# Kernel optimization log

Measured on AMD Instinct MI355X. Metric: run time of the kernel, lower is better.

## Reference

```python
import jax, jax.numpy as jnp
import numpy as np

B, D, E, T = 262144, 128, 8, 3   # batch, input_dim, num_experts, num_tasks
H1, H2, G = 64, 32, 64           # expert hidden dims, gate hidden dim


def setup_inputs() -> dict:
    key = jax.random.key(0)
    ks = jax.random.split(key, 9)
    s = 0.05
    return {
        "x":   jax.random.normal(ks[0], (B, D), dtype=jnp.float32),
        # stacked expert MLP params: D -> H1 (relu) -> H2 (relu)
        "We1": jax.random.normal(ks[1], (E, D, H1), dtype=jnp.float32) * s,
        "be1": jax.random.normal(ks[2], (E, H1), dtype=jnp.float32) * s,
        "We2": jax.random.normal(ks[3], (E, H1, H2), dtype=jnp.float32) * s,
        "be2": jax.random.normal(ks[4], (E, H2), dtype=jnp.float32) * s,
        # stacked gate MLP params: D -> G (relu) -> E (linear, then softmax)
        "Wg1": jax.random.normal(ks[5], (T, D, G), dtype=jnp.float32) * s,
        "bg1": jax.random.normal(ks[6], (T, G), dtype=jnp.float32) * s,
        "Wg2": jax.random.normal(ks[7], (T, G, E), dtype=jnp.float32) * s,
        "bg2": jax.random.normal(ks[8], (T, E), dtype=jnp.float32) * s,
    }


def reference(x, We1, be1, We2, be2, Wg1, bg1, Wg2, bg2):
    # All experts as one batched GEMM chain: [B,E,H1] -> [B,E,H2]
    h1 = jax.nn.relu(jnp.einsum('bd,edh->beh', x, We1) + be1)
    experts_out = jax.nn.relu(jnp.einsum('beh,eho->beo', h1, We2) + be2)  # [B,E,H2]
    # All task gates as one batched GEMM chain: [B,T,E]
    g = jax.nn.relu(jnp.einsum('bd,tdh->bth', x, Wg1) + bg1)
    gate = jax.nn.softmax(jnp.einsum('bth,the->bte', g, Wg2) + bg2, axis=-1)
    # softmax-weighted sum over experts, per task
    out = jnp.einsum('bte,beo->bto', gate, experts_out)  # [B,T,H2]
    return tuple(out[:, t] for t in range(T))
```

## Files before the change

kernel.cpp:

```cpp
#include <hip/hip_runtime.h>

#define BROWS 262144
#define OUT_TASK_F32 8388608

#define WS_L1F 0
#define WS_L2F 196608
#define WS_B1  235520
#define WS_B2  238592

#define H1B 0
#define EOB 24576
#define SGB 40960
#define XSB 42496
#define LDS_TOTAL 50688

typedef __attribute__((ext_vector_type(8))) short bf16x8;
typedef __attribute__((ext_vector_type(4))) float f32x4;
typedef __attribute__((ext_vector_type(2))) unsigned int u32x2;

#define MFMA16(a, b, c) __builtin_amdgcn_mfma_f32_16x16x32_bf16((a), (b), (c), 0, 0, 0)

__device__ __forceinline__ unsigned short f2bf(float f) {
  unsigned int u = __float_as_uint(f);
  return (unsigned short)((u + 0x7FFFu + ((u >> 16) & 1u)) >> 16);
}
__device__ __forceinline__ unsigned int cvtpk(float lo, float hi) {
  unsigned int r;
  asm("v_cvt_pk_bf16_f32 %0, %1, %2" : "=v"(r) : "v"(lo), "v"(hi));
  return r;
}

__global__ void pack_kernel(const float* __restrict__ We1, const float* __restrict__ be1,
                            const float* __restrict__ We2, const float* __restrict__ be2,
                            const float* __restrict__ Wg1, const float* __restrict__ bg1,
                            const float* __restrict__ Wg2, const float* __restrict__ bg2,
                            unsigned char* __restrict__ ws) {
  int idx = blockIdx.x * blockDim.x + threadIdx.x;
  unsigned short* L1F = (unsigned short*)(ws + WS_L1F);
  unsigned short* L2F = (unsigned short*)(ws + WS_L2F);
  float* B1 = (float*)(ws + WS_B1);
  float* B2 = (float*)(ws + WS_B2);
  if (idx < 98304) {
    int j = idx & 7, lane = (idx >> 3) & 63, ks = (idx >> 9) & 3, nt = idx >> 11;
    int k = ks * 32 + ((lane >> 4) << 3) + j;
    int n = nt * 16 + (lane & 15);
    float v = 0.f;
    if (n < 512)      v = We1[((n >> 6) * 128 + k) * 64 + (n & 63)];
    else if (n < 704) v = Wg1[(((n - 512) >> 6) * 128 + k) * 64 + ((n - 512) & 63)];
    L1F[idx] = f2bf(v);
  } else if (idx < 98304 + 19456) {
    int i2 = idx - 98304;
    int j = i2 & 7, lane = (i2 >> 3) & 63, ks = (i2 >> 9) & 1, nt = i2 >> 10;
    int k = ks * 32 + ((lane >> 4) << 3) + j;
    int n = nt * 16 + (lane & 15);
    float v = 0.f;
    if (n < 256) v = We2[((n >> 5) * 64 + k) * 32 + (n & 31)];
    else { int g = n - 256, t = g >> 4, eo = g & 15; if (eo < 8) v = Wg2[(t * 64 + k) * 8 + eo]; }
    L2F[i2] = f2bf(v);
  } else if (idx < 98304 + 19456 + 768) {
    int n = idx - (98304 + 19456);
    float v = 0.f;
    if (n < 512)      v = be1[n];
    else if (n < 704) v = bg1[n - 512];
    B1[n] = v;
  } else if (idx < 98304 + 19456 + 768 + 304) {
    int n = idx - (98304 + 19456 + 768);
    float v = 0.f;
    if (n < 256) v = be2[n];
    else { int g = n - 256, t = g >> 4, eo = g & 15; if (eo < 8) v = bg2[t * 8 + eo]; }
    B2[n] = v;
  }
}

__global__ __launch_bounds__(512, 2) void mmoe_kernel(const float* __restrict__ x,
                                                      const unsigned char* __restrict__ ws,
                                                      float* __restrict__ out) {
  __shared__ unsigned char lds[LDS_TOTAL];

  const int tid = threadIdx.x;
  const int l   = tid & 63;
  const int wid = tid >> 6;
  const int l15 = l & 15;
  const int lhi = l >> 4;
  const int swz = (l15 & 7) << 4;

  const bf16x8* L1F = (const bf16x8*)(ws + WS_L1F);
  const bf16x8* L2F = (const bf16x8*)(ws + WS_L2F);
  const float*  B1  = (const float*)(ws + WS_B1);
  const float*  B2  = (const float*)(ws + WS_B2);

  int ntb[6];
#pragma unroll
  for (int i = 0; i < 6; ++i) ntb[i] = wid * 6 + i;
  if (wid >= 6) {
    int b = wid - 6;
#pragma unroll
    for (int i = 0; i < 4; ++i) ntb[i] = 36 + b * 4 + i;
    ntb[4] = 44 + b * 2; ntb[5] = 45 + b * 2;
  }

  bf16x8 w1f[6][4];
  f32x4 b1v[6];
#pragma unroll
  for (int i = 0; i < 6; ++i) {
#pragma unroll
    for (int ks = 0; ks < 4; ++ks) w1f[i][ks] = L1F[(ntb[i] * 4 + ks) * 64 + l];
    b1v[i] = *(const f32x4*)(B1 + ntb[i] * 16 + lhi * 4);
  }
  bf16x8 w2f[2][2];
  f32x4 b2v[2];
#pragma unroll
  for (int i = 0; i < 2; ++i) {
#pragma unroll
    for (int ks = 0; ks < 2; ++ks) w2f[i][ks] = L2F[((wid * 2 + i) * 2 + ks) * 64 + l];
    b2v[i] = *(const f32x4*)(B2 + wid * 32 + i * 16 + lhi * 4);
  }
  bf16x8 wgf[2];
  f32x4 bgv = (f32x4){0.f, 0.f, 0.f, 0.f};
  if (wid >= 5) {
    int t = wid - 5;
#pragma unroll
    for (int ks = 0; ks < 2; ++ks) wgf[ks] = L2F[((16 + t) * 2 + ks) * 64 + l];
    bgv = *(const f32x4*)(B2 + 256 + t * 16 + lhi * 4);
  }

  const int srow = tid >> 5, sk4 = tid & 31;
  const int rowbase = blockIdx.x * 512;
  const int sswz = (srow & 7) << 4;

  {
    float4 sv = *(const float4*)(x + (size_t)(rowbase + srow) * 128 + sk4 * 4);
    u32x2 p; p[0] = cvtpk(sv.x, sv.y); p[1] = cvtpk(sv.z, sv.w);
    *(u32x2*)(lds + XSB + ((srow * 256 + sk4 * 8) ^ sswz)) = p;
  }
  __syncthreads();

  int cur = 0;
#pragma unroll 1
  for (int it = 0; it < 32; ++it) {
    float4 sv;
    const bool stage = (it + 1 < 32);
    if (stage)
      sv = *(const float4*)(x + (size_t)(rowbase + (it + 1) * 16 + srow) * 128 + sk4 * 4);

    if (it > 0 && wid < 6) {
      int t = wid >> 1, hf = wid & 1;
      f32x4 pA = *(const f32x4*)(lds + SGB + l15 * 96 + t * 32);
      f32x4 pB = *(const f32x4*)(lds + SGB + l15 * 96 + t * 32 + 16);
      f32x4 vac = (f32x4){0.f, 0.f, 0.f, 0.f};
#pragma unroll
      for (int e = 0; e < 4; ++e)
        vac += pA[e] * (*(const f32x4*)(lds + EOB + l15 * 1024 + ((e * 128 + hf * 64 + lhi * 16) ^ swz)));
#pragma unroll
      for (int e = 0; e < 4; ++e)
        vac += pB[e] * (*(const f32x4*)(lds + EOB + l15 * 1024 + (((e + 4) * 128 + hf * 64 + lhi * 16) ^ swz)));
      float* op = out + (size_t)t * OUT_TASK_F32 +
                  (size_t)(rowbase + (it - 1) * 16 + l15) * 32 + hf * 16 + lhi * 4;
      *(float4*)op = (float4){vac[0], vac[1], vac[2], vac[3]};
    }

    bf16x8 xa[4];
#pragma unroll
    for (int ks = 0; ks < 4; ++ks)
      xa[ks] = *(const bf16x8*)(lds + XSB + cur * 4096 + l15 * 256 + ((ks * 64 + lhi * 16) ^ swz));

    f32x4 acc[6];
#pragma unroll
    for (int i = 0; i < 6; ++i) acc[i] = b1v[i];
#pragma unroll
    for (int ks = 0; ks < 4; ++ks)
#pragma unroll
      for (int i = 0; i < 6; ++i)
        acc[i] = MFMA16(w1f[i][ks], xa[ks], acc[i]);

#pragma unroll
    for (int i = 0; i < 6; ++i) {
      float h0 = fmaxf(acc[i][0], 0.f), h1 = fmaxf(acc[i][1], 0.f);
      float h2 = fmaxf(acc[i][2], 0.f), h3 = fmaxf(acc[i][3], 0.f);
      u32x2 p; p[0] = cvtpk(h0, h1); p[1] = cvtpk(h2, h3);
      *(u32x2*)(lds + H1B + l15 * 1536 + ((ntb[i] * 32 + lhi * 8) ^ swz)) = p;
    }
    __syncthreads();

    bf16x8 hb0 = *(const bf16x8*)(lds + H1B + l15 * 1536 + ((wid * 128 + lhi * 16) ^ swz));
    bf16x8 hb1 = *(const bf16x8*)(lds + H1B + l15 * 1536 + ((wid * 128 + 64 + lhi * 16) ^ swz));
    f32x4 a2[2] = {b2v[0], b2v[1]};
#pragma unroll
    for (int i = 0; i < 2; ++i) {
      a2[i] = MFMA16(w2f[i][0], hb0, a2[i]);
      a2[i] = MFMA16(w2f[i][1], hb1, a2[i]);
      f32x4 r;
      r[0] = fmaxf(a2[i][0], 0.f); r[1] = fmaxf(a2[i][1], 0.f);
      r[2] = fmaxf(a2[i][2], 0.f); r[3] = fmaxf(a2[i][3], 0.f);
      *(f32x4*)(lds + EOB + l15 * 1024 + ((wid * 128 + i * 64 + lhi * 16) ^ swz)) = r;
    }

    if (wid >= 5) {
      int t = wid - 5;
      bf16x8 gb0 = *(const bf16x8*)(lds + H1B + l15 * 1536 + ((1024 + t * 128 + lhi * 16) ^ swz));
      bf16x8 gb1 = *(const bf16x8*)(lds + H1B + l15 * 1536 + ((1024 + t * 128 + 64 + lhi * 16) ^ swz));
      f32x4 ag = bgv;
      ag = MFMA16(wgf[0], gb0, ag);
      ag = MFMA16(wgf[1], gb1, ag);
      float s0 = ag[0], s1 = ag[1], s2 = ag[2], s3 = ag[3];
      float o0 = __shfl_xor(s0, 16), o1 = __shfl_xor(s1, 16);
      float o2 = __shfl_xor(s2, 16), o3 = __shfl_xor(s3, 16);
      float m = fmaxf(fmaxf(fmaxf(s0, s1), fmaxf(s2, s3)),
                      fmaxf(fmaxf(o0, o1), fmaxf(o2, o3)));
      float q0 = __expf(s0 - m), q1 = __expf(s1 - m), q2 = __expf(s2 - m), q3 = __expf(s3 - m);
      float ps = q0 + q1 + q2 + q3;
      float inv = 1.f / (ps + __shfl_xor(ps, 16));
      if (lhi < 2)
        *(f32x4*)(lds + SGB + l15 * 96 + t * 32 + lhi * 16) =
            (f32x4){q0 * inv, q1 * inv, q2 * inv, q3 * inv};
    }

    if (stage) {
      u32x2 p; p[0] = cvtpk(sv.x, sv.y); p[1] = cvtpk(sv.z, sv.w);
      *(u32x2*)(lds + XSB + (cur ^ 1) * 4096 + ((srow * 256 + sk4 * 8) ^ sswz)) = p;
    }
    __syncthreads();
    cur ^= 1;
  }

  if (wid < 6) {
    int t = wid >> 1, hf = wid & 1;
    f32x4 pA = *(const f32x4*)(lds + SGB + l15 * 96 + t * 32);
    f32x4 pB = *(const f32x4*)(lds + SGB + l15 * 96 + t * 32 + 16);
    f32x4 vac = (f32x4){0.f, 0.f, 0.f, 0.f};
#pragma unroll
    for (int e = 0; e < 4; ++e)
      vac += pA[e] * (*(const f32x4*)(lds + EOB + l15 * 1024 + ((e * 128 + hf * 64 + lhi * 16) ^ swz)));
#pragma unroll
    for (int e = 0; e < 4; ++e)
      vac += pB[e] * (*(const f32x4*)(lds + EOB + l15 * 1024 + (((e + 4) * 128 + hf * 64 + lhi * 16) ^ swz)));
    float* op = out + (size_t)t * OUT_TASK_F32 +
                (size_t)(rowbase + 31 * 16 + l15) * 32 + hf * 16 + lhi * 4;
    *(float4*)op = (float4){vac[0], vac[1], vac[2], vac[3]};
  }
}

extern "C" void kernel_launch(void* const* d_in, const int* in_sizes, int n_in,
                              void* d_out, int out_size, void* d_ws, size_t ws_size,
                              hipStream_t stream) {
  const float* x   = (const float*)d_in[0];
  const float* We1 = (const float*)d_in[1];
  const float* be1 = (const float*)d_in[2];
  const float* We2 = (const float*)d_in[3];
  const float* be2 = (const float*)d_in[4];
  const float* Wg1 = (const float*)d_in[5];
  const float* bg1 = (const float*)d_in[6];
  const float* Wg2 = (const float*)d_in[7];
  const float* bg2 = (const float*)d_in[8];
  unsigned char* ws = (unsigned char*)d_ws;
  float* out = (float*)d_out;

  pack_kernel<<<465, 256, 0, stream>>>(We1, be1, We2, be2, Wg1, bg1, Wg2, bg2, ws);
  mmoe_kernel<<<512, 512, 0, stream>>>(x, ws, out);
}
```

Baseline: 108.3 us.

## Process two 16-row sub-tiles per iteration to halve barriers per row

Each loop iteration now handles 32 rows as two 16-row MFMA sub-tiles, with the H1, expert-output, gate and x staging buffers all doubled in LDS. The grid drops from 512 to 256 blocks of 1024 rows each, and each thread stages 8 floats of x per iteration. The aim is to amortise the two __syncthreads per iteration and the loop overhead over twice as many rows, and to widen the x loads. In exchange, LDS use roughly doubles to about 99 KB, which may limit occupancy, and 256 blocks may not fill all CUs of the device.

```diff
diff --git a/kernel.cpp b/kernel.cpp
--- a/kernel.cpp
+++ b/kernel.cpp
@@ -9,14 +9,15 @@
 #define WS_B2  238592
 
 #define H1B 0
-#define EOB 24576
-#define SGB 40960
-#define XSB 42496
-#define LDS_TOTAL 50688
+#define EOB 49152
+#define SGB 81920
+#define XSB 84992
+#define LDS_TOTAL 101376
 
 typedef __attribute__((ext_vector_type(8))) short bf16x8;
 typedef __attribute__((ext_vector_type(4))) float f32x4;
 typedef __attribute__((ext_vector_type(2))) unsigned int u32x2;
+typedef __attribute__((ext_vector_type(4))) unsigned int u32x4;
 
 #define MFMA16(a, b, c) __builtin_amdgcn_mfma_f32_16x16x32_bf16((a), (b), (c), 0, 0, 0)
 
@@ -124,100 +125,116 @@
     bgv = *(const f32x4*)(B2 + 256 + t * 16 + lhi * 4);
   }
 
-  const int srow = tid >> 5, sk4 = tid & 31;
-  const int rowbase = blockIdx.x * 512;
-  const int sswz = (srow & 7) << 4;
+  const int r32 = tid >> 4;
+  const int c8  = (tid & 15) * 8;
+  const int sboff = (r32 >> 4) * 4096 + (r32 & 15) * 256 + (((tid & 15) * 16) ^ ((r32 & 7) << 4));
+  const int rowbase = blockIdx.x * 1024;
 
   {
-    float4 sv = *(const float4*)(x + (size_t)(rowbase + srow) * 128 + sk4 * 4);
-    u32x2 p; p[0] = cvtpk(sv.x, sv.y); p[1] = cvtpk(sv.z, sv.w);
-    *(u32x2*)(lds + XSB + ((srow * 256 + sk4 * 8) ^ sswz)) = p;
+    const float* xp = x + (size_t)(rowbase + r32) * 128 + c8;
+    float4 a = *(const float4*)xp, b = *(const float4*)(xp + 4);
+    u32x4 p; p[0] = cvtpk(a.x, a.y); p[1] = cvtpk(a.z, a.w);
+    p[2] = cvtpk(b.x, b.y); p[3] = cvtpk(b.z, b.w);
+    *(u32x4*)(lds + XSB + sboff) = p;
   }
   __syncthreads();
 
   int cur = 0;
 #pragma unroll 1
   for (int it = 0; it < 32; ++it) {
-    float4 sv;
+    float4 sa, sb;
     const bool stage = (it + 1 < 32);
-    if (stage)
-      sv = *(const float4*)(x + (size_t)(rowbase + (it + 1) * 16 + srow) * 128 + sk4 * 4);
+    if (stage) {
+      const float* xp = x + (size_t)(rowbase + (it + 1) * 32 + r32) * 128 + c8;
+      sa = *(const float4*)xp; sb = *(const float4*)(xp + 4);
+    }
 
     if (it > 0 && wid < 6) {
       int t = wid >> 1, hf = wid & 1;
-      f32x4 pA = *(const f32x4*)(lds + SGB + l15 * 96 + t * 32);
-      f32x4 pB = *(const f32x4*)(lds + SGB + l15 * 96 + t * 32 + 16);
-      f32x4 vac = (f32x4){0.f, 0.f, 0.f, 0.f};
-#pragma unroll
-      for (int e = 0; e < 4; ++e)
-        vac += pA[e] * (*(const f32x4*)(lds + EOB + l15 * 1024 + ((e * 128 + hf * 64 + lhi * 16) ^ swz)));
-#pragma unroll
-      for (int e = 0; e < 4; ++e)
-        vac += pB[e] * (*(const f32x4*)(lds + EOB + l15 * 1024 + (((e + 4) * 128 + hf * 64 + lhi * 16) ^ swz)));
-      float* op = out + (size_t)t * OUT_TASK_F32 +
-                  (size_t)(rowbase + (it - 1) * 16 + l15) * 32 + hf * 16 + lhi * 4;
-      *(float4*)op = (float4){vac[0], vac[1], vac[2], vac[3]};
-    }
-
-    bf16x8 xa[4];
-#pragma unroll
-    for (int ks = 0; ks < 4; ++ks)
-      xa[ks] = *(const bf16x8*)(lds + XSB + cur * 4096 + l15 * 256 + ((ks * 64 + lhi * 16) ^ swz));
-
-    f32x4 acc[6];
-#pragma unroll
-    for (int i = 0; i < 6; ++i) acc[i] = b1v[i];
-#pragma unroll
-    for (int ks = 0; ks < 4; ++ks)
-#pragma unroll
-      for (int i = 0; i < 6; ++i)
-        acc[i] = MFMA16(w1f[i][ks], xa[ks], acc[i]);
-
-#pragma unroll
-    for (int i = 0; i < 6; ++i) {
-      float h0 = fmaxf(acc[i][0], 0.f), h1 = fmaxf(acc[i][1], 0.f);
-      float h2 = fmaxf(acc[i][2], 0.f), h3 = fmaxf(acc[i][3], 0.f);
-      u32x2 p; p[0] = cvtpk(h0, h1); p[1] = cvtpk(h2, h3);
-      *(u32x2*)(lds + H1B + l15 * 1536 + ((ntb[i] * 32 + lhi * 8) ^ swz)) = p;
+#pragma unroll
+      for (int m = 0; m < 2; ++m) {
+        f32x4 pA = *(const f32x4*)(lds + SGB + m * 1536 + l15 * 96 + t * 32);
+        f32x4 pB = *(const f32x4*)(lds + SGB + m * 1536 + l15 * 96 + t * 32 + 16);
+        f32x4 vac = (f32x4){0.f, 0.f, 0.f, 0.f};
+#pragma unroll
+        for (int e = 0; e < 4; ++e)
+          vac += pA[e] * (*(const f32x4*)(lds + EOB + m * 16384 + l15 * 1024 +
+                                          ((e * 128 + hf * 64 + lhi * 16) ^ swz)));
+#pragma unroll
+        for (int e = 0; e < 4; ++e)
+          vac += pB[e] * (*(const f32x4*)(lds + EOB + m * 16384 + l15 * 1024 +
+                                          (((e + 4) * 128 + hf * 64 + lhi * 16) ^ swz)));
+        float* op = out + (size_t)t * OUT_TASK_F32 +
+                    (size_t)(rowbase + (it - 1) * 32 + m * 16 + l15) * 32 + hf * 16 + lhi * 4;
+        *(float4*)op = (float4){vac[0], vac[1], vac[2], vac[3]};
+      }
+    }
+
+#pragma unroll
+    for (int m = 0; m < 2; ++m) {
+      bf16x8 xa[4];
+#pragma unroll
+      for (int ks = 0; ks < 4; ++ks)
+        xa[ks] = *(const bf16x8*)(lds + XSB + cur * 8192 + m * 4096 + l15 * 256 +
+                                  ((ks * 64 + lhi * 16) ^ swz));
+      f32x4 acc[6];
+#pragma unroll
+      for (int i = 0; i < 6; ++i) acc[i] = b1v[i];
+#pragma unroll
+      for (int ks = 0; ks < 4; ++ks)
+#pragma unroll
+        for (int i = 0; i < 6; ++i)
+          acc[i] = MFMA16(w1f[i][ks], xa[ks], acc[i]);
+#pragma unroll
+      for (int i = 0; i < 6; ++i) {
+        u32x2 p;
+        p[0] = cvtpk(fmaxf(acc[i][0], 0.f), fmaxf(acc[i][1], 0.f));
+        p[1] = cvtpk(fmaxf(acc[i][2], 0.f), fmaxf(acc[i][3], 0.f));
+        *(u32x2*)(lds + H1B + m * 24576 + l15 * 1536 + ((ntb[i] * 32 + lhi * 8) ^ swz)) = p;
+      }
     }
     __syncthreads();
 
-    bf16x8 hb0 = *(const bf16x8*)(lds + H1B + l15 * 1536 + ((wid * 128 + lhi * 16) ^ swz));
-    bf16x8 hb1 = *(const bf16x8*)(lds + H1B + l15 * 1536 + ((wid * 128 + 64 + lhi * 16) ^ swz));
-    f32x4 a2[2] = {b2v[0], b2v[1]};
-#pragma unroll
-    for (int i = 0; i < 2; ++i) {
-      a2[i] = MFMA16(w2f[i][0], hb0, a2[i]);
-      a2[i] = MFMA16(w2f[i][1], hb1, a2[i]);
-      f32x4 r;
-      r[0] = fmaxf(a2[i][0], 0.f); r[1] = fmaxf(a2[i][1], 0.f);
-      r[2] = fmaxf(a2[i][2], 0.f); r[3] = fmaxf(a2[i][3], 0.f);
-      *(f32x4*)(lds + EOB + l15 * 1024 + ((wid * 128 + i * 64 + lhi * 16) ^ swz)) = r;
-    }
-
-    if (wid >= 5) {
-      int t = wid - 5;
-      bf16x8 gb0 = *(const bf16x8*)(lds + H1B + l15 * 1536 + ((1024 + t * 128 + lhi * 16) ^ swz));
-      bf16x8 gb1 = *(const bf16x8*)(lds + H1B + l15 * 1536 + ((1024 + t * 128 + 64 + lhi * 16) ^ swz));
-      f32x4 ag = bgv;
-      ag = MFMA16(wgf[0], gb0, ag);
-      ag = MFMA16(wgf[1], gb1, ag);
-      float s0 = ag[0], s1 = ag[1], s2 = ag[2], s3 = ag[3];
-      float o0 = __shfl_xor(s0, 16), o1 = __shfl_xor(s1, 16);
-      float o2 = __shfl_xor(s2, 16), o3 = __shfl_xor(s3, 16);
-      float m = fmaxf(fmaxf(fmaxf(s0, s1), fmaxf(s2, s3)),
-                      fmaxf(fmaxf(o0, o1), fmaxf(o2, o3)));
-      float q0 = __expf(s0 - m), q1 = __expf(s1 - m), q2 = __expf(s2 - m), q3 = __expf(s3 - m);
-      float ps = q0 + q1 + q2 + q3;
-      float inv = 1.f / (ps + __shfl_xor(ps, 16));
-      if (lhi < 2)
-        *(f32x4*)(lds + SGB + l15 * 96 + t * 32 + lhi * 16) =
-            (f32x4){q0 * inv, q1 * inv, q2 * inv, q3 * inv};
+#pragma unroll
+    for (int m = 0; m < 2; ++m) {
+      bf16x8 hb0 = *(const bf16x8*)(lds + H1B + m * 24576 + l15 * 1536 + ((wid * 128 + lhi * 16) ^ swz));
+      bf16x8 hb1 = *(const bf16x8*)(lds + H1B + m * 24576 + l15 * 1536 + ((wid * 128 + 64 + lhi * 16) ^ swz));
+      f32x4 a2[2] = {b2v[0], b2v[1]};
+#pragma unroll
+      for (int i = 0; i < 2; ++i) {
+        a2[i] = MFMA16(w2f[i][0], hb0, a2[i]);
+        a2[i] = MFMA16(w2f[i][1], hb1, a2[i]);
+        f32x4 r;
+        r[0] = fmaxf(a2[i][0], 0.f); r[1] = fmaxf(a2[i][1], 0.f);
+        r[2] = fmaxf(a2[i][2], 0.f); r[3] = fmaxf(a2[i][3], 0.f);
+        *(f32x4*)(lds + EOB + m * 16384 + l15 * 1024 + ((wid * 128 + i * 64 + lhi * 16) ^ swz)) = r;
+      }
+
+      if (wid >= 5) {
+        int t = wid - 5;
+        bf16x8 gb0 = *(const bf16x8*)(lds + H1B + m * 24576 + l15 * 1536 + ((1024 + t * 128 + lhi * 16) ^ swz));
+        bf16x8 gb1 = *(const bf16x8*)(lds + H1B + m * 24576 + l15 * 1536 + ((1024 + t * 128 + 64 + lhi * 16) ^ swz));
+        f32x4 ag = bgv;
+        ag = MFMA16(wgf[0], gb0, ag);
+        ag = MFMA16(wgf[1], gb1, ag);
+        float s0 = ag[0], s1 = ag[1], s2 = ag[2], s3 = ag[3];
+        float o0 = __shfl_xor(s0, 16), o1 = __shfl_xor(s1, 16);
+        float o2 = __shfl_xor(s2, 16), o3 = __shfl_xor(s3, 16);
+        float mx = fmaxf(fmaxf(fmaxf(s0, s1), fmaxf(s2, s3)),
+                         fmaxf(fmaxf(o0, o1), fmaxf(o2, o3)));
+        float q0 = __expf(s0 - mx), q1 = __expf(s1 - mx), q2 = __expf(s2 - mx), q3 = __expf(s3 - mx);
+        float ps = q0 + q1 + q2 + q3;
+        float inv = 1.f / (ps + __shfl_xor(ps, 16));
+        if (lhi < 2)
+          *(f32x4*)(lds + SGB + m * 1536 + l15 * 96 + t * 32 + lhi * 16) =
+              (f32x4){q0 * inv, q1 * inv, q2 * inv, q3 * inv};
+      }
     }
 
     if (stage) {
-      u32x2 p; p[0] = cvtpk(sv.x, sv.y); p[1] = cvtpk(sv.z, sv.w);
-      *(u32x2*)(lds + XSB + (cur ^ 1) * 4096 + ((srow * 256 + sk4 * 8) ^ sswz)) = p;
+      u32x4 p; p[0] = cvtpk(sa.x, sa.y); p[1] = cvtpk(sa.z, sa.w);
+      p[2] = cvtpk(sb.x, sb.y); p[3] = cvtpk(sb.z, sb.w);
+      *(u32x4*)(lds + XSB + (cur ^ 1) * 8192 + sboff) = p;
     }
     __syncthreads();
     cur ^= 1;
@@ -225,18 +242,23 @@
 
   if (wid < 6) {
     int t = wid >> 1, hf = wid & 1;
-    f32x4 pA = *(const f32x4*)(lds + SGB + l15 * 96 + t * 32);
-    f32x4 pB = *(const f32x4*)(lds + SGB + l15 * 96 + t * 32 + 16);
-    f32x4 vac = (f32x4){0.f, 0.f, 0.f, 0.f};
-#pragma unroll
-    for (int e = 0; e < 4; ++e)
-      vac += pA[e] * (*(const f32x4*)(lds + EOB + l15 * 1024 + ((e * 128 + hf * 64 + lhi * 16) ^ swz)));
-#pragma unroll
-    for (int e = 0; e < 4; ++e)
-      vac += pB[e] * (*(const f32x4*)(lds + EOB + l15 * 1024 + (((e + 4) * 128 + hf * 64 + lhi * 16) ^ swz)));
-    float* op = out + (size_t)t * OUT_TASK_F32 +
-                (size_t)(rowbase + 31 * 16 + l15) * 32 + hf * 16 + lhi * 4;
-    *(float4*)op = (float4){vac[0], vac[1], vac[2], vac[3]};
+#pragma unroll
+    for (int m = 0; m < 2; ++m) {
+      f32x4 pA = *(const f32x4*)(lds + SGB + m * 1536 + l15 * 96 + t * 32);
+      f32x4 pB = *(const f32x4*)(lds + SGB + m * 1536 + l15 * 96 + t * 32 + 16);
+      f32x4 vac = (f32x4){0.f, 0.f, 0.f, 0.f};
+#pragma unroll
+      for (int e = 0; e < 4; ++e)
+        vac += pA[e] * (*(const f32x4*)(lds + EOB + m * 16384 + l15 * 1024 +
+                                        ((e * 128 + hf * 64 + lhi * 16) ^ swz)));
+#pragma unroll
+      for (int e = 0; e < 4; ++e)
+        vac += pB[e] * (*(const f32x4*)(lds + EOB + m * 16384 + l15 * 1024 +
+                                        (((e + 4) * 128 + hf * 64 + lhi * 16) ^ swz)));
+      float* op = out + (size_t)t * OUT_TASK_F32 +
+                  (size_t)(rowbase + 31 * 32 + m * 16 + l15) * 32 + hf * 16 + lhi * 4;
+      *(float4*)op = (float4){vac[0], vac[1], vac[2], vac[3]};
+    }
   }
 }
 
@@ -256,5 +278,5 @@
   float* out = (float*)d_out;
 
   pack_kernel<<<465, 256, 0, stream>>>(We1, be1, We2, be2, Wg1, bg1, Wg2, bg2, ws);
-  mmoe_kernel<<<512, 512, 0, stream>>>(x, ws, out);
-}
+  mmoe_kernel<<<256, 512, 0, stream>>>(x, ws, out);
+}
```

Result: faster. 100.6 us (-7.1%).
